# Optimization experiments

Measured on AMD Instinct MI355X. Metric: run time of the kernel, lower is better.

## Reference

```python
import jax, jax.numpy as jnp
import numpy as np

B, L, W, C = 16, 200, 64, 128
H_INTRA = 64   # intra_hidden // 2 per direction
H_INTER = 128
EPS = 1e-8


def layer_norm(x, gamma, beta):
    mu = jnp.mean(x, axis=-1, keepdims=True)
    var = jnp.mean(jnp.square(x - mu), axis=-1, keepdims=True)
    return (x - mu) * jax.lax.rsqrt(var + EPS) * gamma + beta


def gru_seq(x, Wk, Uk, b, H):
    """Keras GRU, reset_after=False, recurrent_activation=sigmoid. x: [N,T,D] -> [N,T,H]."""
    xw = jnp.einsum('ntd,dk->ntk', x, Wk) + b  # precompute input projections [N,T,3H]
    def step(h, xw_t):
        z = jax.nn.sigmoid(xw_t[:, :H] + h @ Uk[:, :H])
        r = jax.nn.sigmoid(xw_t[:, H:2 * H] + h @ Uk[:, H:2 * H])
        hh = jnp.tanh(xw_t[:, 2 * H:] + (r * h) @ Uk[:, 2 * H:])
        h = z * h + (1.0 - z) * hh
        return h, h
    h0 = jnp.zeros((x.shape[0], H), x.dtype)
    _, ys = jax.lax.scan(step, h0, jnp.swapaxes(xw, 0, 1))  # [T,N,H]
    return jnp.swapaxes(ys, 0, 1)


def skip_gru_seq(x, Wk, Uk, b, Wp, bp, H):
    """Skip-RNN GRU (Campos et al.): binary update gate u_t conditionally updates state.
    Returns (outputs [N,T,H], gates [N,T,1])."""
    xw = jnp.einsum('ntd,dk->ntk', x, Wk) + b
    def step(carry, xw_t):
        h, ut = carry
        # straight-through binarization of cumulative update prob
        u = ut + jax.lax.stop_gradient(jnp.round(ut) - ut)  # [N,1]
        z = jax.nn.sigmoid(xw_t[:, :H] + h @ Uk[:, :H])
        r = jax.nn.sigmoid(xw_t[:, H:2 * H] + h @ Uk[:, H:2 * H])
        hh = jnp.tanh(xw_t[:, 2 * H:] + (r * h) @ Uk[:, 2 * H:])
        h_new = z * h + (1.0 - z) * hh
        h = u * h_new + (1.0 - u) * h  # skip: copy state when u == 0
        delta = jax.nn.sigmoid(h @ Wp + bp)  # [N,1]
        ut_next = u * delta + (1.0 - u) * (ut + jnp.minimum(delta, 1.0 - ut))
        return (h, ut_next), (h, u)
    N = x.shape[0]
    h0 = jnp.zeros((N, H), x.dtype)
    ut0 = jnp.ones((N, 1), x.dtype)
    _, (ys, us) = jax.lax.scan(step, (h0, ut0), jnp.swapaxes(xw, 0, 1))
    return jnp.swapaxes(ys, 0, 1), jnp.swapaxes(us, 0, 1)


def setup_inputs():
    key = jax.random.key(0)
    ks = jax.random.split(key, 16)
    rn = lambda k, s: jax.random.normal(k, s, dtype=jnp.float32) * 0.05
    z = lambda s: jnp.zeros(s, jnp.float32)
    o = lambda s: jnp.ones(s, jnp.float32)
    return {
        'x': jax.random.normal(ks[0], (B, L, W, C), dtype=jnp.float32),
        'scale': jax.random.uniform(ks[1], (B, L, W, 1), dtype=jnp.float32),
        'Wf': rn(ks[2], (C, 3 * H_INTRA)), 'Uf': rn(ks[3], (H_INTRA, 3 * H_INTRA)), 'bf': z((3 * H_INTRA,)),
        'Wb': rn(ks[4], (C, 3 * H_INTRA)), 'Ub': rn(ks[5], (H_INTRA, 3 * H_INTRA)), 'bb': z((3 * H_INTRA,)),
        'W_intra_fc': rn(ks[6], (2 * H_INTRA, C)), 'b_intra_fc': z((C,)),
        'g_intra': o((C,)), 'beta_intra': z((C,)),
        'Wi': rn(ks[7], (C + 1, 3 * H_INTER)), 'Ui': rn(ks[8], (H_INTER, 3 * H_INTER)), 'bi': z((3 * H_INTER,)),
        'Wp': rn(ks[9], (H_INTER, 1)), 'bp': z((1,)),
        'W_inter_fc': rn(ks[10], (H_INTER, C)), 'b_inter_fc': z((C,)),
        'g_inter': o((C,)), 'beta_inter': z((C,)),
    }


def reference(x, scale, Wf, Uf, bf, Wb, Ub, bb, W_intra_fc, b_intra_fc, g_intra, beta_intra,
              Wi, Ui, bi, Wp, bp, W_inter_fc, b_inter_fc, g_inter, beta_inter):
    # ----- intra path: bidirectional GRU over the width axis -----
    intra_in = x.reshape(B * L, W, C)
    out_f = gru_seq(intra_in, Wf, Uf, bf, H_INTRA)
    out_b = gru_seq(intra_in[:, ::-1, :], Wb, Ub, bb, H_INTRA)[:, ::-1, :]
    intra_rnn_out = jnp.concatenate([out_f, out_b], axis=-1)  # [B*L, W, 2H]
    update_gate_intra = jnp.ones((64, L), jnp.float32)  # skip=0 branch: constant ones
    intra_dense = intra_rnn_out @ W_intra_fc + b_intra_fc  # [B*L, W, C]
    intra_out = x + layer_norm(intra_dense.reshape(B, L, W, C), g_intra, beta_intra)
    # ----- inter path: skip-GRU over the L (time) axis -----
    inter_in = jnp.transpose(intra_out, (0, 2, 1, 3)).reshape(B * W, L, C)
    scale2 = jnp.transpose(scale, (0, 2, 1, 3)).reshape(B * W, L, 1)
    inter_in = jnp.concatenate([inter_in, scale2], axis=-1)  # [B*W, L, C+1]
    inter_rnn_out, gates = skip_gru_seq(inter_in, Wi, Ui, bi, Wp, bp, H_INTER)
    update_gate_inter = gates[:, :, 0]  # [B*W, L]
    inter_dense = (inter_rnn_out @ W_inter_fc + b_inter_fc).reshape(B, W, L, C)
    inter_ln_in = jnp.transpose(inter_dense, (0, 2, 1, 3))  # [B, L, W, C]
    inter_out = intra_out + layer_norm(inter_ln_in, g_inter, beta_inter)
    return inter_out, update_gate_intra, update_gate_inter
```

## Files before the change

kernel.cpp:

```cpp
#include <hip/hip_runtime.h>
#include <cmath>


__device__ __forceinline__ float sigf(float x) { return 1.0f / (1.0f + expf(-x)); }

__global__ __launch_bounds__(256) void k_fill_ones(float* __restrict__ p, int n) {
  int i = blockIdx.x * 256 + threadIdx.x;
  if (i < n) p[i] = 1.0f;
}

enum { MA_X_FWD = 0, MA_X_BWD = 1, MA_INTER = 2 };

template <int MODE>
__global__ __launch_bounds__(256) void k_gemm_xw(
    const float* __restrict__ A0, const float* __restrict__ A1,
    const float* __restrict__ Bm, const float* __restrict__ bias,
    float* __restrict__ Cm, long M0, int N, int K, int KT)
{
  __shared__ float As[16][68];
  __shared__ float Bs[16][68];
  const int tid = threadIdx.x;
  const int tx = tid & 15, ty = tid >> 4;
  const long row0g = M0 + (long)blockIdx.x * 64;
  const int col0 = blockIdx.y * 64;
  const int lr = tid >> 2;
  const int lk4 = (tid & 3) * 4;
  const int bk = tid >> 4;
  const int bc4 = (tid & 15) * 4;
  float acc[4][4];
#pragma unroll
  for (int i = 0; i < 4; ++i)
#pragma unroll
    for (int j = 0; j < 4; ++j) acc[i][j] = 0.f;

  for (int kt = 0; kt < KT; ++kt) {
    const int k0 = kt * 16;
    {
      const long rg = row0g + lr;
      float v0, v1, v2, v3;
      if (MODE == MA_X_FWD) {
        const float4 a4 = *reinterpret_cast<const float4*>(&A0[rg * 128 + k0 + lk4]);
        v0 = a4.x; v1 = a4.y; v2 = a4.z; v3 = a4.w;
      } else if (MODE == MA_X_BWD) {
        const long s = rg >> 6; const int t = (int)(rg & 63);
        const float4 a4 =
            *reinterpret_cast<const float4*>(&A0[(s * 64 + (63 - t)) * 128 + k0 + lk4]);
        v0 = a4.x; v1 = a4.y; v2 = a4.z; v3 = a4.w;
      } else {
        const long n = rg / 200; const int l = (int)(rg - n * 200);
        const long bq = n >> 6; const int w = (int)(n & 63);
        const long rowc = (bq * 200 + l) * 64 + w;
        const long base = rowc * 128;
        float vv[4];
#pragma unroll
        for (int i = 0; i < 4; ++i) {
          const int k = k0 + lk4 + i;
          vv[i] = (k < 128) ? A0[base + k] : ((k == 128) ? A1[rowc] : 0.f);
        }
        v0 = vv[0]; v1 = vv[1]; v2 = vv[2]; v3 = vv[3];
      }
      As[lk4 + 0][lr] = v0;
      As[lk4 + 1][lr] = v1;
      As[lk4 + 2][lr] = v2;
      As[lk4 + 3][lr] = v3;
    }
    {
      const int k = k0 + bk;
      float4 b4 = make_float4(0.f, 0.f, 0.f, 0.f);
      if (k < K) b4 = *reinterpret_cast<const float4*>(&Bm[(long)k * N + col0 + bc4]);
      *reinterpret_cast<float4*>(&Bs[bk][bc4]) = b4;
    }
    __syncthreads();
#pragma unroll
    for (int kk = 0; kk < 16; ++kk) {
      const float4 a4 = *reinterpret_cast<const float4*>(&As[kk][ty * 4]);
      const float4 b4 = *reinterpret_cast<const float4*>(&Bs[kk][tx * 4]);
      const float av[4] = {a4.x, a4.y, a4.z, a4.w};
      const float bv[4] = {b4.x, b4.y, b4.z, b4.w};
#pragma unroll
      for (int i = 0; i < 4; ++i)
#pragma unroll
        for (int j = 0; j < 4; ++j) acc[i][j] = fmaf(av[i], bv[j], acc[i][j]);
    }
    __syncthreads();
  }
  const float4 bi4 = *reinterpret_cast<const float4*>(&bias[col0 + tx * 4]);
  const float bv[4] = {bi4.x, bi4.y, bi4.z, bi4.w};
#pragma unroll
  for (int i = 0; i < 4; ++i) {
    const long rl = (long)blockIdx.x * 64 + ty * 4 + i;
    float4 o;
    o.x = acc[i][0] + bv[0];
    o.y = acc[i][1] + bv[1];
    o.z = acc[i][2] + bv[2];
    o.w = acc[i][3] + bv[3];
    *reinterpret_cast<float4*>(&Cm[rl * (long)N + col0 + tx * 4]) = o;
  }
}

__global__ __launch_bounds__(256, 2) void k_gru_intra(
    const float* __restrict__ xwf, const float* __restrict__ xwb,
    const float* __restrict__ Uf, const float* __restrict__ Ub,
    float* __restrict__ rnn, int nseq)
{
  const int dir = blockIdx.y;
  const float* __restrict__ xw = dir ? xwb : xwf;
  const float* __restrict__ U = dir ? Ub : Uf;
  __shared__ float Us[64 * 192];
  __shared__ float hs[8][64];
  __shared__ float zs[8][64];
  __shared__ float rhs[8][64];
  const int tid = threadIdx.x;
#pragma unroll
  for (int i = 0; i < 12; ++i) {
    *reinterpret_cast<float4*>(&Us[(tid + i * 256) * 4]) =
        *reinterpret_cast<const float4*>(&U[(tid + i * 256) * 4]);
  }
  reinterpret_cast<float*>(hs)[tid] = 0.f;
  reinterpret_cast<float*>(hs)[tid + 256] = 0.f;
  __syncthreads();
  const int sA = tid >> 5;
  const int cA = tid & 31;
  const long s0 = (long)blockIdx.x * 8;
  const long xbase = (s0 + sA) * 64;
  float4 xzr = *reinterpret_cast<const float4*>(&xw[(xbase + 0) * 192 + 4 * cA]);
  float2 xh = *reinterpret_cast<const float2*>(&xw[(xbase + 0) * 192 + 128 + 2 * cA]);
  for (int t = 0; t < 64; ++t) {
    float4 xzr_n = make_float4(0.f, 0.f, 0.f, 0.f);
    float2 xh_n = make_float2(0.f, 0.f);
    if (t < 63) {
      xzr_n = *reinterpret_cast<const float4*>(&xw[(xbase + t + 1) * 192 + 4 * cA]);
      xh_n = *reinterpret_cast<const float2*>(&xw[(xbase + t + 1) * 192 + 128 + 2 * cA]);
    }
    float a0 = 0.f, a1 = 0.f, a2 = 0.f, a3 = 0.f;
#pragma unroll
    for (int k4 = 0; k4 < 16; ++k4) {
      const float4 h4 = *reinterpret_cast<const float4*>(&hs[sA][4 * k4]);
      const float hv[4] = {h4.x, h4.y, h4.z, h4.w};
#pragma unroll
      for (int i = 0; i < 4; ++i) {
        const float4 u4 =
            *reinterpret_cast<const float4*>(&Us[(4 * k4 + i) * 192 + 4 * cA]);
        a0 = fmaf(hv[i], u4.x, a0);
        a1 = fmaf(hv[i], u4.y, a1);
        a2 = fmaf(hv[i], u4.z, a2);
        a3 = fmaf(hv[i], u4.w, a3);
      }
    }
    if (cA < 16) {
      float4 zq;
      zq.x = sigf(xzr.x + a0);
      zq.y = sigf(xzr.y + a1);
      zq.z = sigf(xzr.z + a2);
      zq.w = sigf(xzr.w + a3);
      *reinterpret_cast<float4*>(&zs[sA][4 * cA]) = zq;
    } else {
      const int j0 = 4 * cA - 64;
      const float4 h4 = *reinterpret_cast<const float4*>(&hs[sA][j0]);
      float4 rq;
      rq.x = sigf(xzr.x + a0) * h4.x;
      rq.y = sigf(xzr.y + a1) * h4.y;
      rq.z = sigf(xzr.z + a2) * h4.z;
      rq.w = sigf(xzr.w + a3) * h4.w;
      *reinterpret_cast<float4*>(&rhs[sA][j0]) = rq;
    }
    __syncthreads();
    float b0 = 0.f, b1 = 0.f;
#pragma unroll
    for (int k4 = 0; k4 < 16; ++k4) {
      const float4 r4 = *reinterpret_cast<const float4*>(&rhs[sA][4 * k4]);
      const float rv[4] = {r4.x, r4.y, r4.z, r4.w};
#pragma unroll
      for (int i = 0; i < 4; ++i) {
        const float2 u2 =
            *reinterpret_cast<const float2*>(&Us[(4 * k4 + i) * 192 + 128 + 2 * cA]);
        b0 = fmaf(rv[i], u2.x, b0);
        b1 = fmaf(rv[i], u2.y, b1);
      }
    }
    {
      const int j0 = 2 * cA;
      const float hh0 = tanhf(xh.x + b0);
      const float hh1 = tanhf(xh.y + b1);
      const float z0 = zs[sA][j0], z1 = zs[sA][j0 + 1];
      const float ho0 = hs[sA][j0], ho1 = hs[sA][j0 + 1];
      const float hn0 = z0 * ho0 + (1.f - z0) * hh0;
      const float hn1 = z1 * ho1 + (1.f - z1) * hh1;
      hs[sA][j0] = hn0;
      hs[sA][j0 + 1] = hn1;
      const int tt = dir ? (63 - t) : t;
      float2 st; st.x = hn0; st.y = hn1;
      *reinterpret_cast<float2*>(
          &rnn[((s0 + sA) * 64 + tt) * 128 + dir * 64 + j0]) = st;
    }
    __syncthreads();
    xzr = xzr_n; xh = xh_n;
  }
}

__global__ __launch_bounds__(512, 2) void k_gru_inter(
    const float* __restrict__ xw, const float* __restrict__ Ui,
    const float* __restrict__ Wp, const float* __restrict__ bp,
    float* __restrict__ rnn, float* __restrict__ gates, int chunk_s0)
{
  __shared__ float h_s[4][128];
  __shared__ float rh_s[4][128];
  __shared__ float z_s[4][128];
  __shared__ float pA[4][256];
  __shared__ float pB[3][4][128];
  __shared__ float wp_s[128];
  __shared__ float ut_s[4];
  __shared__ float u_s[4];
  const int tid = threadIdx.x;
  const int ksA = tid >> 8;
  const int cA = tid & 255;
  const int ksB = tid >> 7;
  const int cB = tid & 127;
  const int s0l = blockIdx.x * 4;
  float uzr[64];
#pragma unroll
  for (int k = 0; k < 64; ++k) uzr[k] = Ui[(long)(ksA * 64 + k) * 384 + cA];
  float u3[32];
#pragma unroll
  for (int k = 0; k < 32; ++k) u3[k] = Ui[(long)(ksB * 32 + k) * 384 + 256 + cB];
  reinterpret_cast<float*>(h_s)[tid] = 0.f;
  if (tid < 128) wp_s[tid] = Wp[tid];
  if (tid < 4) { ut_s[tid] = 1.0f; u_s[tid] = 1.0f; }
  const float bp0 = bp[0];
  __syncthreads();
  float xa[4] = {0.f, 0.f, 0.f, 0.f}, xb[4] = {0.f, 0.f, 0.f, 0.f};
  if (ksA == 0) {
#pragma unroll
    for (int s = 0; s < 4; ++s)
      xa[s] = xw[((long)(s0l + s) * 200 + 0) * 384 + cA];
  }
  if (ksB == 0) {
#pragma unroll
    for (int s = 0; s < 4; ++s)
      xb[s] = xw[((long)(s0l + s) * 200 + 0) * 384 + 256 + cB];
  }
  for (int t = 0; t < 200; ++t) {
    float xa_n[4] = {0.f, 0.f, 0.f, 0.f}, xb_n[4] = {0.f, 0.f, 0.f, 0.f};
    if (t < 199) {
      if (ksA == 0) {
#pragma unroll
        for (int s = 0; s < 4; ++s)
          xa_n[s] = xw[((long)(s0l + s) * 200 + t + 1) * 384 + cA];
      }
      if (ksB == 0) {
#pragma unroll
        for (int s = 0; s < 4; ++s)
          xb_n[s] = xw[((long)(s0l + s) * 200 + t + 1) * 384 + 256 + cB];
      }
    }
    float accA[4];
#pragma unroll
    for (int s = 0; s < 4; ++s) {
      float a = 0.f;
#pragma unroll
      for (int k4 = 0; k4 < 16; ++k4) {
        const float4 hv =
            *reinterpret_cast<const float4*>(&h_s[s][ksA * 64 + 4 * k4]);
        a = fmaf(hv.x, uzr[4 * k4 + 0], a);
        a = fmaf(hv.y, uzr[4 * k4 + 1], a);
        a = fmaf(hv.z, uzr[4 * k4 + 2], a);
        a = fmaf(hv.w, uzr[4 * k4 + 3], a);
      }
      accA[s] = a;
    }
    if (ksA == 1) {
#pragma unroll
      for (int s = 0; s < 4; ++s) pA[s][cA] = accA[s];
    }
    __syncthreads();
    if (ksA == 0) {
#pragma unroll
      for (int s = 0; s < 4; ++s) {
        const float pre = xa[s] + accA[s] + pA[s][cA];
        if (cA < 128) {
          z_s[s][cA] = sigf(pre);
        } else {
          const float r = sigf(pre);
          rh_s[s][cA - 128] = r * h_s[s][cA - 128];
        }
      }
    }
    __syncthreads();
    float accB[4];
#pragma unroll
    for (int s = 0; s < 4; ++s) {
      float a = 0.f;
#pragma unroll
      for (int k4 = 0; k4 < 8; ++k4) {
        const float4 rv =
            *reinterpret_cast<const float4*>(&rh_s[s][ksB * 32 + 4 * k4]);
        a = fmaf(rv.x, u3[4 * k4 + 0], a);
        a = fmaf(rv.y, u3[4 * k4 + 1], a);
        a = fmaf(rv.z, u3[4 * k4 + 2], a);
        a = fmaf(rv.w, u3[4 * k4 + 3], a);
      }
      accB[s] = a;
    }
    if (ksB != 0) {
#pragma unroll
      for (int s = 0; s < 4; ++s) pB[ksB - 1][s][cB] = accB[s];
    }
    __syncthreads();
    if (ksB == 0) {
#pragma unroll
      for (int s = 0; s < 4; ++s) {
        const float pre = xb[s] + accB[s] + pB[0][s][cB] + pB[1][s][cB] + pB[2][s][cB];
        const float hh = tanhf(pre);
        const float z = z_s[s][cB];
        const float ho = h_s[s][cB];
        const float hn = z * ho + (1.f - z) * hh;
        const float u = u_s[s];
        const float hq = u * hn + (1.f - u) * ho;
        h_s[s][cB] = hq;
        rnn[((long)(s0l + s) * 200 + t) * 128 + cB] = hq;
      }
    }
    __syncthreads();
    {
      const int wv = tid >> 6, ln = tid & 63;
      if (wv < 4) {
        float p = h_s[wv][ln] * wp_s[ln] + h_s[wv][64 + ln] * wp_s[64 + ln];
        p += __shfl_xor(p, 32, 64);
        p += __shfl_xor(p, 16, 64);
        p += __shfl_xor(p, 8, 64);
        p += __shfl_xor(p, 4, 64);
        p += __shfl_xor(p, 2, 64);
        p += __shfl_xor(p, 1, 64);
        if (ln == 0) {
          const float delta = sigf(p + bp0);
          const float u = u_s[wv], ut = ut_s[wv];
          gates[(long)(chunk_s0 + s0l + wv) * 200 + t] = u;
          const float utn = u * delta + (1.f - u) * (ut + fminf(delta, 1.f - ut));
          ut_s[wv] = utn;
          u_s[wv] = rintf(utn);
        }
      }
    }
    __syncthreads();
#pragma unroll
    for (int s = 0; s < 4; ++s) { xa[s] = xa_n[s]; xb[s] = xb_n[s]; }
  }
}

template <int OM>
__global__ __launch_bounds__(256) void k_fcln(
    const float* __restrict__ A, const float* __restrict__ Wt,
    const float* __restrict__ bias, const float* __restrict__ gamma,
    const float* __restrict__ beta, const float* __restrict__ resid,
    float* __restrict__ dst, long M0)
{
  __shared__ float As[16][36];
  __shared__ float Bs[16][132];
  __shared__ float red0[32][33];
  __shared__ float red1[32][33];
  __shared__ float mu_s[32];
  __shared__ float rs_s[32];
  const int tid = threadIdx.x;
  const int tx = tid & 31, ty = tid >> 5;
  const long r0l = (long)blockIdx.x * 32;
  const int lr = tid >> 3;
  const int lk2 = (tid & 7) * 2;
  const int bkk = tid >> 4;
  const int bc8 = (tid & 15) * 8;
  float acc[4][4];
#pragma unroll
  for (int i = 0; i < 4; ++i)
#pragma unroll
    for (int j = 0; j < 4; ++j) acc[i][j] = 0.f;

  for (int kt = 0; kt < 8; ++kt) {
    const int k0 = kt * 16;
    const float2 a2 = *reinterpret_cast<const float2*>(&A[(r0l + lr) * 128 + k0 + lk2]);
    As[lk2][lr] = a2.x;
    As[lk2 + 1][lr] = a2.y;
    const float4 w0 = *reinterpret_cast<const float4*>(&Wt[(long)(k0 + bkk) * 128 + bc8]);
    const float4 w1 = *reinterpret_cast<const float4*>(&Wt[(long)(k0 + bkk) * 128 + bc8 + 4]);
    *reinterpret_cast<float4*>(&Bs[bkk][bc8]) = w0;
    *reinterpret_cast<float4*>(&Bs[bkk][bc8 + 4]) = w1;
    __syncthreads();
#pragma unroll
    for (int kk = 0; kk < 16; ++kk) {
      const float4 a4 = *reinterpret_cast<const float4*>(&As[kk][ty * 4]);
      const float4 b4 = *reinterpret_cast<const float4*>(&Bs[kk][tx * 4]);
      const float av[4] = {a4.x, a4.y, a4.z, a4.w};
      const float bv[4] = {b4.x, b4.y, b4.z, b4.w};
#pragma unroll
      for (int i = 0; i < 4; ++i)
#pragma unroll
        for (int j = 0; j < 4; ++j) acc[i][j] = fmaf(av[i], bv[j], acc[i][j]);
    }
    __syncthreads();
  }
  {
    const float4 bb4 = *reinterpret_cast<const float4*>(&bias[tx * 4]);
    const float bv[4] = {bb4.x, bb4.y, bb4.z, bb4.w};
#pragma unroll
    for (int i = 0; i < 4; ++i)
#pragma unroll
      for (int j = 0; j < 4; ++j) acc[i][j] += bv[j];
  }
#pragma unroll
  for (int i = 0; i < 4; ++i) {
    const float s = acc[i][0] + acc[i][1] + acc[i][2] + acc[i][3];
    const float q = acc[i][0] * acc[i][0] + acc[i][1] * acc[i][1] +
                    acc[i][2] * acc[i][2] + acc[i][3] * acc[i][3];
    red0[ty * 4 + i][tx] = s;
    red1[ty * 4 + i][tx] = q;
  }
  __syncthreads();
  if (tid < 32) {
    float s = 0.f, q = 0.f;
#pragma unroll
    for (int j = 0; j < 32; ++j) { s += red0[tid][j]; q += red1[tid][j]; }
    const float mu = s * (1.0f / 128.0f);
    const float var = q * (1.0f / 128.0f) - mu * mu;
    mu_s[tid] = mu;
    rs_s[tid] = 1.0f / sqrtf(var + 1e-8f);
  }
  __syncthreads();
  const float4 g4 = *reinterpret_cast<const float4*>(&gamma[tx * 4]);
  const float4 be4 = *reinterpret_cast<const float4*>(&beta[tx * 4]);
#pragma unroll
  for (int i = 0; i < 4; ++i) {
    const int rloc = ty * 4 + i;
    const long rg = M0 + r0l + rloc;
    long off;
    if (OM == 0) {
      off = rg * 128 + tx * 4;
    } else {
      const long n = rg / 200; const int l = (int)(rg - n * 200);
      const long bq = n >> 6; const int w = (int)(n & 63);
      off = ((bq * 200 + l) * 64 + w) * 128 + tx * 4;
    }
    const float4 r4 = *reinterpret_cast<const float4*>(&resid[off]);
    const float mu = mu_s[rloc], rs = rs_s[rloc];
    float4 o;
    o.x = (acc[i][0] - mu) * rs * g4.x + be4.x + r4.x;
    o.y = (acc[i][1] - mu) * rs * g4.y + be4.y + r4.y;
    o.z = (acc[i][2] - mu) * rs * g4.z + be4.z + r4.z;
    o.w = (acc[i][3] - mu) * rs * g4.w + be4.w + r4.w;
    *reinterpret_cast<float4*>(&dst[off]) = o;
  }
}

extern "C" void kernel_launch(void* const* d_in, const int* in_sizes, int n_in,
                              void* d_out, int out_size, void* d_ws, size_t ws_size,
                              hipStream_t stream)
{
  (void)in_sizes; (void)n_in; (void)out_size;
  const float* x    = (const float*)d_in[0];
  const float* scl  = (const float*)d_in[1];
  const float* Wf   = (const float*)d_in[2];
  const float* Uf   = (const float*)d_in[3];
  const float* bf   = (const float*)d_in[4];
  const float* Wb   = (const float*)d_in[5];
  const float* Ub   = (const float*)d_in[6];
  const float* bb   = (const float*)d_in[7];
  const float* Wfc1 = (const float*)d_in[8];
  const float* bfc1 = (const float*)d_in[9];
  const float* gam1 = (const float*)d_in[10];
  const float* bet1 = (const float*)d_in[11];
  const float* Wi   = (const float*)d_in[12];
  const float* Ui   = (const float*)d_in[13];
  const float* bi   = (const float*)d_in[14];
  const float* Wp   = (const float*)d_in[15];
  const float* bp   = (const float*)d_in[16];
  const float* Wfc2 = (const float*)d_in[17];
  const float* bfc2 = (const float*)d_in[18];
  const float* gam2 = (const float*)d_in[19];
  const float* bet2 = (const float*)d_in[20];

  float* outp  = (float*)d_out;
  float* io    = outp;
  float* onesp = outp + 26214400L;
  float* gates = outp + 26214400L + 12800L;
  float* ws    = (float*)d_ws;
  const long wsf = (long)(ws_size / sizeof(float));

  k_fill_ones<<<50, 256, 0, stream>>>(onesp, 12800);

  long cnI = (wsf / 32768L) & ~7L;
  if (cnI > 3200) cnI = 3200;
  if (cnI < 8) cnI = 8;
  for (long s0 = 0; s0 < 3200; s0 += cnI) {
    const long cn = (3200 - s0 < cnI) ? (3200 - s0) : cnI;
    float* xwf = ws;
    float* xwb = ws + cn * 12288L;
    float* rnn = ws + cn * 24576L;
    const long M = cn * 64;
    dim3 gg((unsigned)(M / 64), 3);
    k_gemm_xw<MA_X_FWD><<<gg, 256, 0, stream>>>(x, nullptr, Wf, bf, xwf, s0 * 64, 192, 128, 8);
    k_gemm_xw<MA_X_BWD><<<gg, 256, 0, stream>>>(x, nullptr, Wb, bb, xwb, s0 * 64, 192, 128, 8);
    dim3 gr((unsigned)(cn / 8), 2);
    k_gru_intra<<<gr, 256, 0, stream>>>(xwf, xwb, Uf, Ub, rnn, (int)cn);
    k_fcln<0><<<(unsigned)(M / 32), 256, 0, stream>>>(rnn, Wfc1, bfc1, gam1, bet1, x, io, s0 * 64);
  }

  long cnE = (wsf / 102400L) & ~7L;
  if (cnE > 1024) cnE = 1024;
  if (cnE < 8) cnE = 8;
  for (long s0 = 0; s0 < 1024; s0 += cnE) {
    const long cn = (1024 - s0 < cnE) ? (1024 - s0) : cnE;
    float* xwi = ws;
    float* rnn = ws + cn * 76800L;
    const long M = cn * 200;
    dim3 gg((unsigned)(M / 64), 6);
    k_gemm_xw<MA_INTER><<<gg, 256, 0, stream>>>(io, scl, Wi, bi, xwi, s0 * 200, 384, 129, 9);
    k_gru_inter<<<(unsigned)(cn / 4), 512, 0, stream>>>(xwi, Ui, Wp, bp, rnn, gates, (int)s0);
    k_fcln<1><<<(unsigned)(M / 32), 256, 0, stream>>>(rnn, Wfc2, bfc2, gam2, bet2, io, outp, s0 * 200);
  }
}
```

Baseline: 2.045 ms.

## Restructure inter skip-GRU to two sequences per block with time-major layout

The inter-path GRU kernel now handles 2 sequences per 512-thread block instead of 4, which gives 512 blocks. It keeps the candidate-gate recurrent weights in XOR-swizzled shared memory instead of registers, and cuts the partial-sum exchanges and barriers per step by reducing with wave shuffles. The input-projection buffer, RNN output and FC/LayerNorm indexing switch to a time-major layout, chunked along time with hidden and gate state carried through workspace. The aim is more parallelism across the GPU and less barrier and shared-memory traffic per recurrent step. The cost is heavy shared-memory use per block (64KB of weights) and extra state save/restore when the time axis is chunked.

```diff
diff --git a/kernel.cpp b/kernel.cpp
--- a/kernel.cpp
+++ b/kernel.cpp
@@ -47,9 +47,9 @@
             *reinterpret_cast<const float4*>(&A0[(s * 64 + (63 - t)) * 128 + k0 + lk4]);
         v0 = a4.x; v1 = a4.y; v2 = a4.z; v3 = a4.w;
       } else {
-        const long n = rg / 200; const int l = (int)(rg - n * 200);
-        const long bq = n >> 6; const int w = (int)(n & 63);
-        const long rowc = (bq * 200 + l) * 64 + w;
+        const int n = (int)(rg & 1023);
+        const int l = (int)(rg >> 10);
+        const long rowc = ((long)(n >> 6) * 200 + l) * 64 + (n & 63);
         const long base = rowc * 128;
         float vv[4];
 #pragma unroll
@@ -198,152 +198,146 @@
   }
 }
 
-__global__ __launch_bounds__(512, 2) void k_gru_inter(
+__global__ __launch_bounds__(512, 4) void k_gru_inter2(
     const float* __restrict__ xw, const float* __restrict__ Ui,
     const float* __restrict__ Wp, const float* __restrict__ bp,
-    float* __restrict__ rnn, float* __restrict__ gates, int chunk_s0)
+    float* __restrict__ rnn, float* __restrict__ gates,
+    float* __restrict__ hstate, float* __restrict__ ustate,
+    int t0, int nt)
 {
-  __shared__ float h_s[4][128];
-  __shared__ float rh_s[4][128];
-  __shared__ float z_s[4][128];
-  __shared__ float pA[4][256];
-  __shared__ float pB[3][4][128];
+  __shared__ float Uh[128 * 128];
+  __shared__ float h_s[2][128];
+  __shared__ float z_s[2][128];
+  __shared__ float rh_s[2][128];
   __shared__ float wp_s[128];
-  __shared__ float ut_s[4];
-  __shared__ float u_s[4];
+  __shared__ float pred[2][4];
+  __shared__ float ut_s[2];
+  __shared__ float u_s[2];
   const int tid = threadIdx.x;
-  const int ksA = tid >> 8;
-  const int cA = tid & 255;
-  const int ksB = tid >> 7;
-  const int cB = tid & 127;
-  const int s0l = blockIdx.x * 4;
+  const int w = tid >> 6, lane = tid & 63, half = lane >> 5, lcol = lane & 31;
+  const int n0 = blockIdx.x * 2;
+  const int colA = w * 32 + lcol;
+  const int ksA = half;
+  const int seqB = w >> 2;
+  const int colB = (w & 3) * 32 + lcol;
+  const int ksB = half;
+
   float uzr[64];
 #pragma unroll
-  for (int k = 0; k < 64; ++k) uzr[k] = Ui[(long)(ksA * 64 + k) * 384 + cA];
-  float u3[32];
-#pragma unroll
-  for (int k = 0; k < 32; ++k) u3[k] = Ui[(long)(ksB * 32 + k) * 384 + 256 + cB];
-  reinterpret_cast<float*>(h_s)[tid] = 0.f;
+  for (int k = 0; k < 64; ++k) uzr[k] = Ui[(long)(ksA * 64 + k) * 384 + colA];
+
+  for (int idx = tid; idx < 16384; idx += 512) {
+    const int k = idx >> 7, c = idx & 127;
+    const float v = Ui[(long)k * 384 + 256 + c];
+    Uh[c * 128 + (((k >> 2) ^ (c & 31)) << 2) + (k & 3)] = v;
+  }
+  if (tid < 256) {
+    const int s = tid >> 7, c = tid & 127;
+    h_s[s][c] = (t0 == 0) ? 0.f : hstate[(long)(n0 + s) * 128 + c];
+  }
   if (tid < 128) wp_s[tid] = Wp[tid];
-  if (tid < 4) { ut_s[tid] = 1.0f; u_s[tid] = 1.0f; }
+  if (tid < 2) {
+    ut_s[tid] = (t0 == 0) ? 1.0f : ustate[n0 + tid];
+    u_s[tid] = (t0 == 0) ? 1.0f : ustate[1024 + n0 + tid];
+  }
   const float bp0 = bp[0];
   __syncthreads();
-  float xa[4] = {0.f, 0.f, 0.f, 0.f}, xb[4] = {0.f, 0.f, 0.f, 0.f};
-  if (ksA == 0) {
-#pragma unroll
-    for (int s = 0; s < 4; ++s)
-      xa[s] = xw[((long)(s0l + s) * 200 + 0) * 384 + cA];
-  }
-  if (ksB == 0) {
-#pragma unroll
-    for (int s = 0; s < 4; ++s)
-      xb[s] = xw[((long)(s0l + s) * 200 + 0) * 384 + 256 + cB];
-  }
-  for (int t = 0; t < 200; ++t) {
-    float xa_n[4] = {0.f, 0.f, 0.f, 0.f}, xb_n[4] = {0.f, 0.f, 0.f, 0.f};
-    if (t < 199) {
-      if (ksA == 0) {
-#pragma unroll
-        for (int s = 0; s < 4; ++s)
-          xa_n[s] = xw[((long)(s0l + s) * 200 + t + 1) * 384 + cA];
+
+  float xa0 = 0.f, xa1 = 0.f, xb0 = 0.f;
+  if (lane < 32) {
+    xa0 = xw[(long)n0 * 384 + colA];
+    xa1 = xw[(long)(n0 + 1) * 384 + colA];
+    xb0 = xw[(long)(n0 + seqB) * 384 + 256 + colB];
+  }
+
+  for (int dl = 0; dl < nt; ++dl) {
+    const int dn = (dl + 1 < nt) ? dl + 1 : dl;
+    float xa0n = 0.f, xa1n = 0.f, xbn = 0.f;
+    if (lane < 32) {
+      xa0n = xw[((long)dn * 1024 + n0) * 384 + colA];
+      xa1n = xw[((long)dn * 1024 + n0 + 1) * 384 + colA];
+      xbn = xw[((long)dn * 1024 + n0 + seqB) * 384 + 256 + colB];
+    }
+    float a0 = 0.f, a1 = 0.f;
+    const int hb = ksA * 64;
+#pragma unroll
+    for (int k4 = 0; k4 < 16; ++k4) {
+      const float4 h0 = *reinterpret_cast<const float4*>(&h_s[0][hb + 4 * k4]);
+      const float4 h1 = *reinterpret_cast<const float4*>(&h_s[1][hb + 4 * k4]);
+      a0 = fmaf(h0.x, uzr[4 * k4 + 0], a0);
+      a0 = fmaf(h0.y, uzr[4 * k4 + 1], a0);
+      a0 = fmaf(h0.z, uzr[4 * k4 + 2], a0);
+      a0 = fmaf(h0.w, uzr[4 * k4 + 3], a0);
+      a1 = fmaf(h1.x, uzr[4 * k4 + 0], a1);
+      a1 = fmaf(h1.y, uzr[4 * k4 + 1], a1);
+      a1 = fmaf(h1.z, uzr[4 * k4 + 2], a1);
+      a1 = fmaf(h1.w, uzr[4 * k4 + 3], a1);
+    }
+    a0 += __shfl_xor(a0, 32);
+    a1 += __shfl_xor(a1, 32);
+    if (lane < 32) {
+      const float p0 = xa0 + a0;
+      const float p1 = xa1 + a1;
+      if (colA < 128) {
+        z_s[0][colA] = sigf(p0);
+        z_s[1][colA] = sigf(p1);
+      } else {
+        const int c = colA - 128;
+        rh_s[0][c] = sigf(p0) * h_s[0][c];
+        rh_s[1][c] = sigf(p1) * h_s[1][c];
       }
-      if (ksB == 0) {
-#pragma unroll
-        for (int s = 0; s < 4; ++s)
-          xb_n[s] = xw[((long)(s0l + s) * 200 + t + 1) * 384 + 256 + cB];
-      }
-    }
-    float accA[4];
-#pragma unroll
-    for (int s = 0; s < 4; ++s) {
-      float a = 0.f;
-#pragma unroll
-      for (int k4 = 0; k4 < 16; ++k4) {
-        const float4 hv =
-            *reinterpret_cast<const float4*>(&h_s[s][ksA * 64 + 4 * k4]);
-        a = fmaf(hv.x, uzr[4 * k4 + 0], a);
-        a = fmaf(hv.y, uzr[4 * k4 + 1], a);
-        a = fmaf(hv.z, uzr[4 * k4 + 2], a);
-        a = fmaf(hv.w, uzr[4 * k4 + 3], a);
-      }
-      accA[s] = a;
-    }
-    if (ksA == 1) {
-#pragma unroll
-      for (int s = 0; s < 4; ++s) pA[s][cA] = accA[s];
-    }
-    __syncthreads();
-    if (ksA == 0) {
-#pragma unroll
-      for (int s = 0; s < 4; ++s) {
-        const float pre = xa[s] + accA[s] + pA[s][cA];
-        if (cA < 128) {
-          z_s[s][cA] = sigf(pre);
-        } else {
-          const float r = sigf(pre);
-          rh_s[s][cA - 128] = r * h_s[s][cA - 128];
-        }
-      }
-    }
-    __syncthreads();
-    float accB[4];
-#pragma unroll
-    for (int s = 0; s < 4; ++s) {
-      float a = 0.f;
-#pragma unroll
-      for (int k4 = 0; k4 < 8; ++k4) {
-        const float4 rv =
-            *reinterpret_cast<const float4*>(&rh_s[s][ksB * 32 + 4 * k4]);
-        a = fmaf(rv.x, u3[4 * k4 + 0], a);
-        a = fmaf(rv.y, u3[4 * k4 + 1], a);
-        a = fmaf(rv.z, u3[4 * k4 + 2], a);
-        a = fmaf(rv.w, u3[4 * k4 + 3], a);
-      }
-      accB[s] = a;
-    }
-    if (ksB != 0) {
-#pragma unroll
-      for (int s = 0; s < 4; ++s) pB[ksB - 1][s][cB] = accB[s];
-    }
-    __syncthreads();
-    if (ksB == 0) {
-#pragma unroll
-      for (int s = 0; s < 4; ++s) {
-        const float pre = xb[s] + accB[s] + pB[0][s][cB] + pB[1][s][cB] + pB[2][s][cB];
-        const float hh = tanhf(pre);
-        const float z = z_s[s][cB];
-        const float ho = h_s[s][cB];
-        const float hn = z * ho + (1.f - z) * hh;
-        const float u = u_s[s];
-        const float hq = u * hn + (1.f - u) * ho;
-        h_s[s][cB] = hq;
-        rnn[((long)(s0l + s) * 200 + t) * 128 + cB] = hq;
-      }
-    }
-    __syncthreads();
-    {
-      const int wv = tid >> 6, ln = tid & 63;
-      if (wv < 4) {
-        float p = h_s[wv][ln] * wp_s[ln] + h_s[wv][64 + ln] * wp_s[64 + ln];
-        p += __shfl_xor(p, 32, 64);
-        p += __shfl_xor(p, 16, 64);
-        p += __shfl_xor(p, 8, 64);
-        p += __shfl_xor(p, 4, 64);
-        p += __shfl_xor(p, 2, 64);
-        p += __shfl_xor(p, 1, 64);
-        if (ln == 0) {
-          const float delta = sigf(p + bp0);
-          const float u = u_s[wv], ut = ut_s[wv];
-          gates[(long)(chunk_s0 + s0l + wv) * 200 + t] = u;
-          const float utn = u * delta + (1.f - u) * (ut + fminf(delta, 1.f - ut));
-          ut_s[wv] = utn;
-          u_s[wv] = rintf(utn);
-        }
-      }
-    }
-    __syncthreads();
-#pragma unroll
-    for (int s = 0; s < 4; ++s) { xa[s] = xa_n[s]; xb[s] = xb_n[s]; }
+    }
+    __syncthreads();
+    float b = 0.f;
+    const int rb = ksB * 64;
+#pragma unroll
+    for (int k4 = 0; k4 < 16; ++k4) {
+      const float4 r4 = *reinterpret_cast<const float4*>(&rh_s[seqB][rb + 4 * k4]);
+      const int chunk = ((ksB << 4) + k4) ^ (colB & 31);
+      const float4 u4 = *reinterpret_cast<const float4*>(&Uh[colB * 128 + (chunk << 2)]);
+      b = fmaf(r4.x, u4.x, b);
+      b = fmaf(r4.y, u4.y, b);
+      b = fmaf(r4.z, u4.z, b);
+      b = fmaf(r4.w, u4.w, b);
+    }
+    b += __shfl_xor(b, 32);
+    if (lane < 32) {
+      const float pre = xb0 + b;
+      const float hh = tanhf(pre);
+      const float z = z_s[seqB][colB];
+      const float ho = h_s[seqB][colB];
+      const float hn = z * ho + (1.f - z) * hh;
+      const float u = u_s[seqB];
+      const float hq = u * hn + (1.f - u) * ho;
+      rnn[((long)dl * 1024 + n0 + seqB) * 128 + colB] = hq;
+      h_s[seqB][colB] = hq;
+      float p = hq * wp_s[colB];
+      p += __shfl_xor(p, 16);
+      p += __shfl_xor(p, 8);
+      p += __shfl_xor(p, 4);
+      p += __shfl_xor(p, 2);
+      p += __shfl_xor(p, 1);
+      if (lcol == 0) pred[seqB][w & 3] = p;
+    }
+    __syncthreads();
+    if (tid < 2) {
+      const float pp = pred[tid][0] + pred[tid][1] + pred[tid][2] + pred[tid][3];
+      const float delta = sigf(pp + bp0);
+      const float u = u_s[tid], ut = ut_s[tid];
+      gates[(long)(n0 + tid) * 200 + t0 + dl] = u;
+      const float utn = u * delta + (1.f - u) * (ut + fminf(delta, 1.f - ut));
+      ut_s[tid] = utn;
+      u_s[tid] = rintf(utn);
+    }
+    xa0 = xa0n; xa1 = xa1n; xb0 = xbn;
+  }
+  if (tid < 256) {
+    const int s = tid >> 7, c = tid & 127;
+    hstate[(long)(n0 + s) * 128 + c] = h_s[s][c];
+  }
+  if (tid < 2) {
+    ustate[n0 + tid] = ut_s[tid];
+    ustate[1024 + n0 + tid] = u_s[tid];
   }
 }
 
@@ -433,9 +427,9 @@
     if (OM == 0) {
       off = rg * 128 + tx * 4;
     } else {
-      const long n = rg / 200; const int l = (int)(rg - n * 200);
-      const long bq = n >> 6; const int w = (int)(n & 63);
-      off = ((bq * 200 + l) * 64 + w) * 128 + tx * 4;
+      const int n = (int)(rg & 1023);
+      const int l = (int)(rg >> 10);
+      off = (((long)(n >> 6) * 200 + l) * 64 + (n & 63)) * 128 + tx * 4;
     }
     const float4 r4 = *reinterpret_cast<const float4*>(&resid[off]);
     const float mu = mu_s[rloc], rs = rs_s[rloc];
@@ -501,17 +495,23 @@
     k_fcln<0><<<(unsigned)(M / 32), 256, 0, stream>>>(rnn, Wfc1, bfc1, gam1, bet1, x, io, s0 * 64);
   }
 
-  long cnE = (wsf / 102400L) & ~7L;
-  if (cnE > 1024) cnE = 1024;
-  if (cnE < 8) cnE = 8;
-  for (long s0 = 0; s0 < 1024; s0 += cnE) {
-    const long cn = (1024 - s0 < cnE) ? (1024 - s0) : cnE;
-    float* xwi = ws;
-    float* rnn = ws + cn * 76800L;
-    const long M = cn * 200;
-    dim3 gg((unsigned)(M / 64), 6);
-    k_gemm_xw<MA_INTER><<<gg, 256, 0, stream>>>(io, scl, Wi, bi, xwi, s0 * 200, 384, 129, 9);
-    k_gru_inter<<<(unsigned)(cn / 4), 512, 0, stream>>>(xwi, Ui, Wp, bp, rnn, gates, (int)s0);
-    k_fcln<1><<<(unsigned)(M / 32), 256, 0, stream>>>(rnn, Wfc2, bfc2, gam2, bet2, io, outp, s0 * 200);
+  const long per_t = 1024L * 384 + 1024L * 128;
+  const long state_f = 1024L * 128 + 2048L;
+  long nt_alloc = (wsf - state_f) / per_t;
+  if (nt_alloc > 200) nt_alloc = 200;
+  if (nt_alloc < 1) nt_alloc = 1;
+  float* xwi    = ws;
+  float* rnnI   = ws + nt_alloc * 1024L * 384;
+  float* hstate = rnnI + nt_alloc * 1024L * 128;
+  float* ustate = hstate + 1024L * 128;
+
+  for (long t0 = 0; t0 < 200; t0 += nt_alloc) {
+    const int nt = (int)((200 - t0 < nt_alloc) ? (200 - t0) : nt_alloc);
+    dim3 gg((unsigned)(16 * nt), 6);
+    k_gemm_xw<MA_INTER><<<gg, 256, 0, stream>>>(io, scl, Wi, bi, xwi, t0 * 1024, 384, 129, 9);
+    k_gru_inter2<<<512, 512, 0, stream>>>(xwi, Ui, Wp, bp, rnnI, gates, hstate, ustate,
+                                          (int)t0, nt);
+    k_fcln<1><<<(unsigned)(32 * nt), 256, 0, stream>>>(rnnI, Wfc2, bfc2, gam2, bet2, io, outp,
+                                                       t0 * 1024);
   }
 }
```

After: 2.112 ms. 3.3% more time.
